# Performance work log

Measured on AMD Instinct MI355X. Metric: run time of the kernel, lower is better.

The kernel has to match this reference:

```python
import jax, jax.numpy as jnp
import numpy as np

B, S, DIM = 2, 2048, 2048
H = 16
NOPE, ROPE, VHD = 128, 64, 128
QKHD = NOPE + ROPE  # 192
KV_RANK = 512
EPS = 1e-5


def _rope(x, cos, sin):
    # x: [B,S,H,ROPE]; cos/sin: [S,ROPE//2]; torch view_as_complex pairs (even,odd)
    xr = x.reshape(*x.shape[:-1], ROPE // 2, 2)
    a, b = xr[..., 0], xr[..., 1]
    c = cos[None, :, None, :]
    s = sin[None, :, None, :]
    ra = a * c - b * s
    rb = a * s + b * c
    return jnp.stack([ra, rb], axis=-1).reshape(x.shape)


def setup_inputs() -> dict:
    key = jax.random.key(0)
    ks = jax.random.split(key, 12)
    std = 0.02
    x = jax.random.normal(ks[0], (B, S, DIM), jnp.float32)
    wq_w = jax.random.normal(ks[1], (DIM, H * QKHD), jnp.float32) * std
    wq_b = jnp.zeros((H * QKHD,), jnp.float32)
    wkv_a_w = jax.random.normal(ks[2], (DIM, KV_RANK + H * ROPE), jnp.float32) * std
    wkv_a_b = jnp.zeros((KV_RANK + H * ROPE,), jnp.float32)
    kvn_g = jnp.ones((KV_RANK,), jnp.float32)
    kvn_b = jnp.zeros((KV_RANK,), jnp.float32)
    wk_w = jax.random.normal(ks[3], (KV_RANK, H * NOPE), jnp.float32) * std
    wk_b = jnp.zeros((H * NOPE,), jnp.float32)
    wv_w = jax.random.normal(ks[4], (KV_RANK, H * VHD), jnp.float32) * std
    wv_b = jnp.zeros((H * VHD,), jnp.float32)
    wo_w = jax.random.normal(ks[5], (H * VHD, DIM), jnp.float32) * std
    wo_b = jnp.zeros((DIM,), jnp.float32)
    # RoPE tables: theta = pos / 10000^(2j/ROPE)
    inv_freq = 1.0 / (10000.0 ** (jnp.arange(0, ROPE, 2, dtype=jnp.float32) / ROPE))
    ang = jnp.arange(S, dtype=jnp.float32)[:, None] * inv_freq[None, :]  # [S, ROPE//2]
    cos, sin = jnp.cos(ang), jnp.sin(ang)
    mask = jnp.tril(jnp.ones((S, S), dtype=bool))
    return {"x": x, "wq_w": wq_w, "wq_b": wq_b, "wkv_a_w": wkv_a_w, "wkv_a_b": wkv_a_b,
            "kvn_g": kvn_g, "kvn_b": kvn_b, "wk_w": wk_w, "wk_b": wk_b,
            "wv_w": wv_w, "wv_b": wv_b, "wo_w": wo_w, "wo_b": wo_b,
            "cos": cos, "sin": sin, "mask": mask}


def reference(x, wq_w, wq_b, wkv_a_w, wkv_a_b, kvn_g, kvn_b, wk_w, wk_b,
              wv_w, wv_b, wo_w, wo_b, cos, sin, mask):
    # query projection (q_lora_rank == 0 path)
    q = x @ wq_w + wq_b                              # [B,S,H*QKHD]
    # low-rank kv: first H*ROPE dims are per-head k_rope, last KV_RANK is latent
    kv = x @ wkv_a_w + wkv_a_b                       # [B,S,KV_RANK+H*ROPE]
    k_rope = kv[..., : H * ROPE]
    c = kv[..., H * ROPE:]                           # latent [B,S,KV_RANK]
    mu = jnp.mean(c, axis=-1, keepdims=True)
    var = jnp.mean(jnp.square(c - mu), axis=-1, keepdims=True)
    c = (c - mu) / jnp.sqrt(var + EPS) * kvn_g + kvn_b
    k_nope = c @ wk_w + wk_b                         # [B,S,H*NOPE]
    v = c @ wv_w + wv_b                              # [B,S,H*VHD]
    # faithful to original: concat flat then view into heads
    k = jnp.concatenate([k_nope, k_rope], axis=-1).reshape(B, S, H, QKHD)
    q = q.reshape(B, S, H, QKHD)
    v = v.reshape(B, S, H, VHD)
    # RoPE on trailing ROPE dims
    q = jnp.concatenate([q[..., :NOPE], _rope(q[..., NOPE:], cos, sin)], axis=-1)
    k = jnp.concatenate([k[..., :NOPE], _rope(k[..., NOPE:], cos, sin)], axis=-1)
    scale = QKHD ** -0.5
    scores = jnp.einsum('bqhd,bkhd->bhqk', q, k) * scale
    scores = jnp.where(mask[None, None, :, :], scores, -jnp.inf)
    attn = jax.nn.softmax(scores, axis=-1)
    out = jnp.einsum('bhqk,bkhd->bqhd', attn, v).reshape(B, S, H * VHD)
    return out @ wo_w + wo_b
```

## Files before the change

### kernel.cpp

```cpp
#include <hip/hip_runtime.h>
#include <hip/hip_bf16.h>
#include <stdint.h>

#define B_ 2
#define S_ 2048
#define DIM_ 2048
#define H_ 16
#define M_ (B_*S_)

typedef __bf16 bf16x8 __attribute__((ext_vector_type(8)));
typedef float f32x4 __attribute__((ext_vector_type(4)));
typedef __hip_bfloat16 bf16;

__device__ __forceinline__ void async_copy16(const bf16* gsrc, bf16* ldst) {
  __builtin_amdgcn_global_load_lds((const __attribute__((address_space(1))) uint32_t*)gsrc,
                                   (__attribute__((address_space(3))) uint32_t*)ldst, 16, 0, 0);
}

__global__ void cvt_bf16_kernel(const float* __restrict__ in, bf16* __restrict__ out, int n) {
  int i = (blockIdx.x * 256 + threadIdx.x) * 4;
  if (i >= n) return;
  float4 v = *(const float4*)(in + i);
  bf16 o[4] = {__float2bfloat16(v.x), __float2bfloat16(v.y),
               __float2bfloat16(v.z), __float2bfloat16(v.w)};
  *(ushort4*)(out + i) = *(ushort4*)o;
}

__global__ void transpose_cvt_kernel(const float* __restrict__ W, bf16* __restrict__ Wt,
                                     int K, int N) {
  __shared__ float tile[32][33];
  int n0 = blockIdx.x * 32;
  int k0 = blockIdx.y * 32;
  int tx = threadIdx.x, ty = threadIdx.y;
  #pragma unroll
  for (int i = 0; i < 4; i++)
    tile[ty + i*8][tx] = W[(size_t)(k0 + ty + i*8) * N + n0 + tx];
  __syncthreads();
  #pragma unroll
  for (int i = 0; i < 4; i++)
    Wt[(size_t)(n0 + ty + i*8) * K + k0 + tx] = __float2bfloat16(tile[tx][ty + i*8]);
}

template <typename OutT, int MODE>
__global__ void __launch_bounds__(256) gemm_bt_kernel(
    const bf16* __restrict__ A, const bf16* __restrict__ Bt,
    const float* __restrict__ bias, const float* __restrict__ bias2,
    OutT* __restrict__ C, bf16* __restrict__ C2, bf16* __restrict__ C3,
    int M, int N, int K,
    const float* __restrict__ cosT, const float* __restrict__ sinT) {
  __shared__ bf16 As[128 * 32];
  __shared__ bf16 Bs[128 * 32];
  const int tid = threadIdx.x;
  const int wid = tid >> 6;
  const int lane = tid & 63;
  const int g = lane >> 4;
  const int c = lane & 15;

  int bx = blockIdx.x, by = blockIdx.y;
  {
    int gx = gridDim.x;
    int nwg = gx * gridDim.y;
    if ((nwg & 7) == 0) {
      int flat = by * gx + bx;
      int swz = (flat & 7) * (nwg >> 3) + (flat >> 3);
      bx = swz % gx;
      by = swz / gx;
    }
  }
  const int row0 = by * 128;
  const int col0 = bx * 128;
  const int wr = (wid >> 1) * 64;
  const int wc = (wid & 1) * 64;

  f32x4 acc[4][4] = {};

  const int srow = wid * 32 + (lane >> 2);
  const int scol = (lane & 3) * 8;
  const bf16* ga0 = A  + (size_t)(row0 + srow) * K + scol;
  const bf16* gb0 = Bt + (size_t)(col0 + srow) * K + scol;
  bf16* la0 = &As[(wid * 32) * 32];
  bf16* la1 = &As[(wid * 32 + 16) * 32];
  bf16* lb0 = &Bs[(wid * 32) * 32];
  bf16* lb1 = &Bs[(wid * 32 + 16) * 32];

  for (int k0 = 0; k0 < K; k0 += 32) {
    async_copy16(ga0 + k0, la0);
    async_copy16(ga0 + (size_t)16 * K + k0, la1);
    async_copy16(gb0 + k0, lb0);
    async_copy16(gb0 + (size_t)16 * K + k0, lb1);
    __syncthreads();
    bf16x8 af[4], bfr[4];
    #pragma unroll
    for (int i = 0; i < 4; i++) {
      af[i]  = *(const bf16x8*)&As[(wr + i*16 + c) * 32 + g*8];
      bfr[i] = *(const bf16x8*)&Bs[(wc + i*16 + c) * 32 + g*8];
    }
    #pragma unroll
    for (int mi = 0; mi < 4; mi++)
      #pragma unroll
      for (int ni = 0; ni < 4; ni++)
        acc[mi][ni] = __builtin_amdgcn_mfma_f32_16x16x32_bf16(af[mi], bfr[ni], acc[mi][ni], 0, 0, 0);
    __syncthreads();
  }

  if constexpr (MODE == 0) {
    #pragma unroll
    for (int mi = 0; mi < 4; mi++) {
      int row = row0 + wr + mi*16 + g*4;
      #pragma unroll
      for (int ni = 0; ni < 4; ni++) {
        int col = col0 + wc + ni*16 + c;
        float bv = bias[col];
        #pragma unroll
        for (int r = 0; r < 4; r++)
          C[(size_t)(row + r) * N + col] = acc[mi][ni][r] + bv;
      }
    }
  } else {
    auto rope_write = [&](bf16* __restrict__ dst, size_t obase, int s, int d,
                          float val[4], float scale) {
      if (d >= 128) {
        const int pp = (d - 128) >> 1;
        const bool even = (c & 1) == 0;
        #pragma unroll
        for (int r = 0; r < 4; r++) {
          float partner = __shfl_xor(val[r], 1);
          float a  = even ? val[r] : partner;
          float bb = even ? partner : val[r];
          float ct = cosT[(s + r) * 32 + pp], st = sinT[(s + r) * 32 + pp];
          float o = even ? (a * ct - bb * st) : (a * st + bb * ct);
          dst[obase + (size_t)r * 192] = __float2bfloat16(o * scale);
        }
      } else {
        #pragma unroll
        for (int r = 0; r < 4; r++)
          dst[obase + (size_t)r * 192] = __float2bfloat16(val[r] * scale);
      }
    };

    #pragma unroll
    for (int mi = 0; mi < 4; mi++) {
      int row = row0 + wr + mi*16 + g*4;
      int s = row & (S_ - 1);
      int b = row >> 11;
      #pragma unroll
      for (int ni = 0; ni < 4; ni++) {
        int col = col0 + wc + ni*16 + c;
        float val[4];
        if constexpr (MODE == 6) {
          if (col < 3072) {
            float bv = bias[col];
            #pragma unroll
            for (int r = 0; r < 4; r++) val[r] = acc[mi][ni][r] + bv;
            int h = col / 192;
            int d = col - h * 192;
            size_t obase = ((size_t)(b * H_ + h) * S_ + s) * 192 + d;
            rope_write((bf16*)C, obase, s, d, val, 0.07216878364870323f);
          } else {
            int cc = col - 3072;
            float bv = bias2[cc];
            #pragma unroll
            for (int r = 0; r < 4; r++) val[r] = acc[mi][ni][r] + bv;
            if (cc < 1024) {
              int flat = 2048 + cc;
              int h = flat / 192;
              int d = flat - h * 192;
              size_t obase = ((size_t)(b * H_ + h) * S_ + s) * 192 + d;
              rope_write(C2, obase, s, d, val, 1.0f);
            } else {
              #pragma unroll
              for (int r = 0; r < 4; r++)
                C3[(size_t)(row + r) * 512 + (cc - 1024)] = __float2bfloat16(val[r]);
            }
          }
        } else {
          if (col < 2048) {
            float bv = bias[col];
            #pragma unroll
            for (int r = 0; r < 4; r++) val[r] = acc[mi][ni][r] + bv;
            int h = col / 192;
            int d = col - h * 192;
            size_t obase = ((size_t)(b * H_ + h) * S_ + s) * 192 + d;
            rope_write((bf16*)C, obase, s, d, val, 1.0f);
          } else {
            int cc = col - 2048;
            float bv = bias2[cc];
            bf16 tmp[4];
            #pragma unroll
            for (int r = 0; r < 4; r++) tmp[r] = __float2bfloat16(acc[mi][ni][r] + bv);
            size_t idx = ((size_t)(b * H_ + (cc >> 7)) * 128 + (cc & 127)) * S_ + s;
            *(ushort4*)&C2[idx] = *(ushort4*)tmp;
          }
        }
      }
    }
  }
}

__global__ void __launch_bounds__(256) layernorm_kernel(
    const bf16* __restrict__ craw,
    const float* __restrict__ gamma, const float* __restrict__ beta,
    bf16* __restrict__ cn) {
  int row = blockIdx.x * 4 + (threadIdx.x >> 6);
  int lane = threadIdx.x & 63;
  bf16x8 v = *(const bf16x8*)(craw + (size_t)row * 512 + lane * 8);
  float f[8], sum = 0.f, sq = 0.f;
  #pragma unroll
  for (int j = 0; j < 8; j++) { f[j] = (float)v[j]; sum += f[j]; sq += f[j]*f[j]; }
  #pragma unroll
  for (int d = 1; d < 64; d <<= 1) {
    sum += __shfl_xor(sum, d);
    sq  += __shfl_xor(sq, d);
  }
  float mu = sum * (1.f/512.f);
  float var = sq * (1.f/512.f) - mu*mu;
  float rstd = rsqrtf(var + 1e-5f);
  bf16x8 ov;
  #pragma unroll
  for (int j = 0; j < 8; j++) {
    int col = lane*8 + j;
    float o = (f[j] - mu) * rstd * gamma[col] + beta[col];
    ov[j] = (__bf16)o;
  }
  *(bf16x8*)(cn + (size_t)row * 512 + lane * 8) = ov;
}

__global__ void __launch_bounds__(256) flash_attn_kernel(
    const bf16* __restrict__ Qa, const bf16* __restrict__ Ka,
    const bf16* __restrict__ Vt, bf16* __restrict__ Oa) {
  __shared__ bf16 Ks[64 * 200];
  __shared__ bf16 Vs[128 * 72];
  __shared__ bf16 Ps[4][16 * 72];
  const int tid = threadIdx.x;
  const int wid = tid >> 6, lane = tid & 63;
  const int g = lane >> 4, c = lane & 15;
  const int bh = blockIdx.y;
  const int qt = gridDim.x - 1 - blockIdx.x;
  const int q0 = qt * 64;
  const int qw = q0 + wid * 16;
  const float NEG_INF = -__builtin_inff();

  bf16x8 qf[6];
  {
    const bf16* qrow = Qa + ((size_t)bh * S_ + qw + c) * 192;
    #pragma unroll
    for (int t = 0; t < 6; t++) qf[t] = *(const bf16x8*)(qrow + t*32 + g*8);
  }
  float m = NEG_INF, lsum = 0.f;
  f32x4 o[8] = {};

  const int kr = tid >> 2, kpart = tid & 3;
  const int vdv = tid >> 1, vhalf = tid & 1;

  for (int kt = 0; kt <= qt; kt++) {
    const int kv0 = kt * 64;
    {
      const bf16* src = Ka + ((size_t)bh * S_ + kv0 + kr) * 192;
      #pragma unroll
      for (int j = 0; j < 6; j++) {
        int col = (kpart + 4*j) * 8;
        *(bf16x8*)&Ks[kr * 200 + col] = *(const bf16x8*)(src + col);
      }
      const bf16* vsrc = Vt + ((size_t)bh * 128 + vdv) * S_ + kv0;
      #pragma unroll
      for (int j = 0; j < 4; j++) {
        int col = (vhalf*4 + j) * 8;
        *(bf16x8*)&Vs[vdv * 72 + col] = *(const bf16x8*)(vsrc + col);
      }
    }
    __syncthreads();

    f32x4 sc[4] = {};
    #pragma unroll
    for (int mb = 0; mb < 4; mb++) {
      #pragma unroll
      for (int t = 0; t < 6; t++) {
        bf16x8 kf = *(const bf16x8*)&Ks[(mb*16 + c) * 200 + t*32 + g*8];
        sc[mb] = __builtin_amdgcn_mfma_f32_16x16x32_bf16(kf, qf[t], sc[mb], 0, 0, 0);
      }
    }
    if (kt == qt) {
      #pragma unroll
      for (int mb = 0; mb < 4; mb++)
        #pragma unroll
        for (int r = 0; r < 4; r++)
          if (kv0 + mb*16 + g*4 + r > qw + c) sc[mb][r] = NEG_INF;
    }
    float pm = NEG_INF;
    #pragma unroll
    for (int mb = 0; mb < 4; mb++)
      #pragma unroll
      for (int r = 0; r < 4; r++) pm = fmaxf(pm, sc[mb][r]);
    pm = fmaxf(pm, __shfl_xor(pm, 16));
    pm = fmaxf(pm, __shfl_xor(pm, 32));
    const float newm = fmaxf(m, pm);
    const float alpha = __expf(m - newm);
    float rs = 0.f;
    float pv[4][4];
    #pragma unroll
    for (int mb = 0; mb < 4; mb++)
      #pragma unroll
      for (int r = 0; r < 4; r++) { pv[mb][r] = __expf(sc[mb][r] - newm); rs += pv[mb][r]; }
    rs += __shfl_xor(rs, 16);
    rs += __shfl_xor(rs, 32);
    lsum = lsum * alpha + rs;
    m = newm;
    #pragma unroll
    for (int mb = 0; mb < 4; mb++) {
      bf16 w[4];
      #pragma unroll
      for (int r = 0; r < 4; r++) w[r] = __float2bfloat16(pv[mb][r]);
      *(ushort4*)&Ps[wid][c * 72 + mb*16 + g*4] = *(ushort4*)w;
    }
    __syncthreads();
    float ar[4];
    #pragma unroll
    for (int r = 0; r < 4; r++) ar[r] = __shfl(alpha, 20*g + r);
    #pragma unroll
    for (int nb = 0; nb < 8; nb++)
      #pragma unroll
      for (int r = 0; r < 4; r++) o[nb][r] *= ar[r];
    #pragma unroll
    for (int t2 = 0; t2 < 2; t2++) {
      bf16x8 pa = *(const bf16x8*)&Ps[wid][c * 72 + t2*32 + g*8];
      #pragma unroll
      for (int nb = 0; nb < 8; nb++) {
        bf16x8 vf = *(const bf16x8*)&Vs[(nb*16 + c) * 72 + t2*32 + g*8];
        o[nb] = __builtin_amdgcn_mfma_f32_16x16x32_bf16(pa, vf, o[nb], 0, 0, 0);
      }
    }
    __syncthreads();
  }

  float lr[4];
  #pragma unroll
  for (int r = 0; r < 4; r++) lr[r] = 1.f / __shfl(lsum, 20*g + r);
  const int b = bh >> 4, h = bh & 15;
  #pragma unroll
  for (int nb = 0; nb < 8; nb++) {
    #pragma unroll
    for (int r = 0; r < 4; r++) {
      int srow = qw + g*4 + r;
      int dv = nb*16 + c;
      Oa[(((size_t)(b * S_ + srow)) * H_ + h) * 128 + dv] = __float2bfloat16(o[nb][r] * lr[r]);
    }
  }
}

extern "C" void kernel_launch(void* const* d_in, const int* in_sizes, int n_in,
                              void* d_out, int out_size, void* d_ws, size_t ws_size,
                              hipStream_t stream) {
  const float* x     = (const float*)d_in[0];
  const float* wq_w  = (const float*)d_in[1];
  const float* wq_b  = (const float*)d_in[2];
  const float* wkv_w = (const float*)d_in[3];
  const float* wkv_b = (const float*)d_in[4];
  const float* kvn_g = (const float*)d_in[5];
  const float* kvn_b = (const float*)d_in[6];
  const float* wk_w  = (const float*)d_in[7];
  const float* wk_b  = (const float*)d_in[8];
  const float* wv_w  = (const float*)d_in[9];
  const float* wv_b  = (const float*)d_in[10];
  const float* wo_w  = (const float*)d_in[11];
  const float* wo_b  = (const float*)d_in[12];
  const float* cosT  = (const float*)d_in[13];
  const float* sinT  = (const float*)d_in[14];
  float* out = (float*)d_out;
  (void)in_sizes; (void)n_in; (void)out_size; (void)ws_size;

  char* p = (char*)d_ws;
  auto alloc = [&](size_t elems) { bf16* r = (bf16*)p; p += elems * 2; return r; };
  bf16* xb      = alloc((size_t)M_ * 2048);
  bf16* wqkv_t  = alloc((size_t)4608 * 2048);
  bf16* wkv2_t  = alloc((size_t)4096 * 512);
  bf16* wo_t    = alloc((size_t)2048 * 2048);
  bf16* c_raw   = alloc((size_t)M_ * 512);
  bf16* cn      = alloc((size_t)M_ * 512);
  bf16* q_at    = alloc((size_t)M_ * 3072);
  bf16* k_at    = alloc((size_t)M_ * 3072);
  bf16* v_at    = alloc((size_t)M_ * 2048);
  bf16* att_o   = alloc((size_t)M_ * 2048);

  cvt_bf16_kernel<<<dim3((M_*2048)/1024), 256, 0, stream>>>(x, xb, M_*2048);
  transpose_cvt_kernel<<<dim3(3072/32, 2048/32), dim3(32,8), 0, stream>>>(wq_w,  wqkv_t,                      2048, 3072);
  transpose_cvt_kernel<<<dim3(1536/32, 2048/32), dim3(32,8), 0, stream>>>(wkv_w, wqkv_t + (size_t)3072*2048, 2048, 1536);
  transpose_cvt_kernel<<<dim3(2048/32, 512/32),  dim3(32,8), 0, stream>>>(wk_w,  wkv2_t,                     512,  2048);
  transpose_cvt_kernel<<<dim3(2048/32, 512/32),  dim3(32,8), 0, stream>>>(wv_w,  wkv2_t + (size_t)2048*512,  512,  2048);
  transpose_cvt_kernel<<<dim3(2048/32, 2048/32), dim3(32,8), 0, stream>>>(wo_w,  wo_t,                       2048, 2048);
  gemm_bt_kernel<bf16,6><<<dim3(4608/128, M_/128), 256, 0, stream>>>(
      xb, wqkv_t, wq_b, wkv_b, q_at, k_at, c_raw, M_, 4608, 2048, cosT, sinT);
  layernorm_kernel<<<dim3(M_/4), 256, 0, stream>>>(c_raw, kvn_g, kvn_b, cn);
  gemm_bt_kernel<bf16,7><<<dim3(4096/128, M_/128), 256, 0, stream>>>(
      cn, wkv2_t, wk_b, wv_b, k_at, v_at, nullptr, M_, 4096, 512, cosT, sinT);
  flash_attn_kernel<<<dim3(S_/64, B_*H_), 256, 0, stream>>>(q_at, k_at, v_at, att_o);
  gemm_bt_kernel<float,0><<<dim3(2048/128, M_/128), 256, 0, stream>>>(
      att_o, wo_t, wo_b, nullptr, out, nullptr, nullptr, M_, 2048, 2048, nullptr, nullptr);
}
```

Measured before the change: 581.3 us.

## Enlarge flash-attention query tile to 128 rows and prefetch K/V through registers

Each attention block now handles 128 query rows, with every wave owning two 16-row groups, so each K/V tile loaded into LDS is reused by twice as many queries. The next K/V tile is loaded from global memory into registers while the current tile is computed, then written to LDS between barriers. The intra-loop barrier between P store and PV matmul is dropped, and launch bounds request two blocks per CU. The cost is higher register pressure from doubled accumulators and staging registers, and half as many blocks in the grid.

```diff
diff --git a/kernel.cpp b/kernel.cpp
--- a/kernel.cpp
+++ b/kernel.cpp
@@ -225,124 +225,146 @@
   *(bf16x8*)(cn + (size_t)row * 512 + lane * 8) = ov;
 }
 
-__global__ void __launch_bounds__(256) flash_attn_kernel(
+__global__ void __launch_bounds__(256, 2) flash_attn_kernel(
     const bf16* __restrict__ Qa, const bf16* __restrict__ Ka,
     const bf16* __restrict__ Vt, bf16* __restrict__ Oa) {
   __shared__ bf16 Ks[64 * 200];
   __shared__ bf16 Vs[128 * 72];
-  __shared__ bf16 Ps[4][16 * 72];
+  __shared__ bf16 Ps[4][32 * 72];
   const int tid = threadIdx.x;
   const int wid = tid >> 6, lane = tid & 63;
   const int g = lane >> 4, c = lane & 15;
   const int bh = blockIdx.y;
   const int qt = gridDim.x - 1 - blockIdx.x;
-  const int q0 = qt * 64;
-  const int qw = q0 + wid * 16;
+  const int q0 = qt * 128;
+  const int qw = q0 + wid * 32;
   const float NEG_INF = -__builtin_inff();
 
-  bf16x8 qf[6];
-  {
-    const bf16* qrow = Qa + ((size_t)bh * S_ + qw + c) * 192;
-    #pragma unroll
-    for (int t = 0; t < 6; t++) qf[t] = *(const bf16x8*)(qrow + t*32 + g*8);
-  }
-  float m = NEG_INF, lsum = 0.f;
-  f32x4 o[8] = {};
+  bf16x8 qf[2][6];
+  #pragma unroll
+  for (int rg = 0; rg < 2; rg++) {
+    const bf16* qrow = Qa + ((size_t)bh * S_ + qw + rg*16 + c) * 192;
+    #pragma unroll
+    for (int t = 0; t < 6; t++) qf[rg][t] = *(const bf16x8*)(qrow + t*32 + g*8);
+  }
+  float m[2] = {NEG_INF, NEG_INF}, lsum[2] = {0.f, 0.f};
+  f32x4 o[2][8] = {};
 
   const int kr = tid >> 2, kpart = tid & 3;
   const int vdv = tid >> 1, vhalf = tid & 1;
 
-  for (int kt = 0; kt <= qt; kt++) {
+  bf16x8 kst[6], vst[4];
+  const int nkt = 2*qt + 2;
+
+  auto load_regs = [&](int kt) {
+    const bf16* src = Ka + ((size_t)bh * S_ + kt*64 + kr) * 192;
+    #pragma unroll
+    for (int j = 0; j < 6; j++) kst[j] = *(const bf16x8*)(src + (kpart + 4*j) * 8);
+    const bf16* vsrc = Vt + ((size_t)bh * 128 + vdv) * S_ + kt*64;
+    #pragma unroll
+    for (int j = 0; j < 4; j++) vst[j] = *(const bf16x8*)(vsrc + (vhalf*4 + j) * 8);
+  };
+  auto write_lds = [&]() {
+    #pragma unroll
+    for (int j = 0; j < 6; j++) *(bf16x8*)&Ks[kr * 200 + (kpart + 4*j) * 8] = kst[j];
+    #pragma unroll
+    for (int j = 0; j < 4; j++) *(bf16x8*)&Vs[vdv * 72 + (vhalf*4 + j) * 8] = vst[j];
+  };
+
+  load_regs(0);
+  write_lds();
+  __syncthreads();
+
+  for (int kt = 0; kt < nkt; kt++) {
     const int kv0 = kt * 64;
-    {
-      const bf16* src = Ka + ((size_t)bh * S_ + kv0 + kr) * 192;
-      #pragma unroll
-      for (int j = 0; j < 6; j++) {
-        int col = (kpart + 4*j) * 8;
-        *(bf16x8*)&Ks[kr * 200 + col] = *(const bf16x8*)(src + col);
-      }
-      const bf16* vsrc = Vt + ((size_t)bh * 128 + vdv) * S_ + kv0;
-      #pragma unroll
-      for (int j = 0; j < 4; j++) {
-        int col = (vhalf*4 + j) * 8;
-        *(bf16x8*)&Vs[vdv * 72 + col] = *(const bf16x8*)(vsrc + col);
-      }
-    }
-    __syncthreads();
-
-    f32x4 sc[4] = {};
-    #pragma unroll
-    for (int mb = 0; mb < 4; mb++) {
-      #pragma unroll
-      for (int t = 0; t < 6; t++) {
-        bf16x8 kf = *(const bf16x8*)&Ks[(mb*16 + c) * 200 + t*32 + g*8];
-        sc[mb] = __builtin_amdgcn_mfma_f32_16x16x32_bf16(kf, qf[t], sc[mb], 0, 0, 0);
-      }
-    }
-    if (kt == qt) {
+    if (kt + 1 < nkt) load_regs(kt + 1);
+
+    #pragma unroll
+    for (int rg = 0; rg < 2; rg++) {
+      const int qbase = qw + rg * 16;
+      if (kv0 > qbase + 15) continue;
+
+      f32x4 sc[4] = {};
+      #pragma unroll
+      for (int mb = 0; mb < 4; mb++) {
+        #pragma unroll
+        for (int t = 0; t < 6; t++) {
+          bf16x8 kf = *(const bf16x8*)&Ks[(mb*16 + c) * 200 + t*32 + g*8];
+          sc[mb] = __builtin_amdgcn_mfma_f32_16x16x32_bf16(kf, qf[rg][t], sc[mb], 0, 0, 0);
+        }
+      }
+      if (kv0 + 63 > qbase) {
+        #pragma unroll
+        for (int mb = 0; mb < 4; mb++)
+          #pragma unroll
+          for (int r = 0; r < 4; r++)
+            if (kv0 + mb*16 + g*4 + r > qbase + c) sc[mb][r] = NEG_INF;
+      }
+      float pm = NEG_INF;
       #pragma unroll
       for (int mb = 0; mb < 4; mb++)
         #pragma unroll
-        for (int r = 0; r < 4; r++)
-          if (kv0 + mb*16 + g*4 + r > qw + c) sc[mb][r] = NEG_INF;
-    }
-    float pm = NEG_INF;
-    #pragma unroll
-    for (int mb = 0; mb < 4; mb++)
-      #pragma unroll
-      for (int r = 0; r < 4; r++) pm = fmaxf(pm, sc[mb][r]);
-    pm = fmaxf(pm, __shfl_xor(pm, 16));
-    pm = fmaxf(pm, __shfl_xor(pm, 32));
-    const float newm = fmaxf(m, pm);
-    const float alpha = __expf(m - newm);
-    float rs = 0.f;
-    float pv[4][4];
-    #pragma unroll
-    for (int mb = 0; mb < 4; mb++)
-      #pragma unroll
-      for (int r = 0; r < 4; r++) { pv[mb][r] = __expf(sc[mb][r] - newm); rs += pv[mb][r]; }
-    rs += __shfl_xor(rs, 16);
-    rs += __shfl_xor(rs, 32);
-    lsum = lsum * alpha + rs;
-    m = newm;
-    #pragma unroll
-    for (int mb = 0; mb < 4; mb++) {
-      bf16 w[4];
-      #pragma unroll
-      for (int r = 0; r < 4; r++) w[r] = __float2bfloat16(pv[mb][r]);
-      *(ushort4*)&Ps[wid][c * 72 + mb*16 + g*4] = *(ushort4*)w;
-    }
-    __syncthreads();
-    float ar[4];
-    #pragma unroll
-    for (int r = 0; r < 4; r++) ar[r] = __shfl(alpha, 20*g + r);
-    #pragma unroll
-    for (int nb = 0; nb < 8; nb++)
-      #pragma unroll
-      for (int r = 0; r < 4; r++) o[nb][r] *= ar[r];
-    #pragma unroll
-    for (int t2 = 0; t2 < 2; t2++) {
-      bf16x8 pa = *(const bf16x8*)&Ps[wid][c * 72 + t2*32 + g*8];
-      #pragma unroll
-      for (int nb = 0; nb < 8; nb++) {
-        bf16x8 vf = *(const bf16x8*)&Vs[(nb*16 + c) * 72 + t2*32 + g*8];
-        o[nb] = __builtin_amdgcn_mfma_f32_16x16x32_bf16(pa, vf, o[nb], 0, 0, 0);
-      }
-    }
-    __syncthreads();
-  }
-
-  float lr[4];
-  #pragma unroll
-  for (int r = 0; r < 4; r++) lr[r] = 1.f / __shfl(lsum, 20*g + r);
+        for (int r = 0; r < 4; r++) pm = fmaxf(pm, sc[mb][r]);
+      pm = fmaxf(pm, __shfl_xor(pm, 16));
+      pm = fmaxf(pm, __shfl_xor(pm, 32));
+      const float newm = fmaxf(m[rg], pm);
+      const float alpha = __expf(m[rg] - newm);
+      float rs = 0.f;
+      float pv[4][4];
+      #pragma unroll
+      for (int mb = 0; mb < 4; mb++)
+        #pragma unroll
+        for (int r = 0; r < 4; r++) { pv[mb][r] = __expf(sc[mb][r] - newm); rs += pv[mb][r]; }
+      rs += __shfl_xor(rs, 16);
+      rs += __shfl_xor(rs, 32);
+      lsum[rg] = lsum[rg] * alpha + rs;
+      m[rg] = newm;
+      #pragma unroll
+      for (int mb = 0; mb < 4; mb++) {
+        bf16 w[4];
+        #pragma unroll
+        for (int r = 0; r < 4; r++) w[r] = __float2bfloat16(pv[mb][r]);
+        *(ushort4*)&Ps[wid][(rg*16 + c) * 72 + mb*16 + g*4] = *(ushort4*)w;
+      }
+      float ar[4];
+      #pragma unroll
+      for (int r = 0; r < 4; r++) ar[r] = __shfl(alpha, 20*g + r);
+      #pragma unroll
+      for (int nb = 0; nb < 8; nb++)
+        #pragma unroll
+        for (int r = 0; r < 4; r++) o[rg][nb][r] *= ar[r];
+      #pragma unroll
+      for (int t2 = 0; t2 < 2; t2++) {
+        bf16x8 pa = *(const bf16x8*)&Ps[wid][(rg*16 + c) * 72 + t2*32 + g*8];
+        #pragma unroll
+        for (int nb = 0; nb < 8; nb++) {
+          bf16x8 vf = *(const bf16x8*)&Vs[(nb*16 + c) * 72 + t2*32 + g*8];
+          o[rg][nb] = __builtin_amdgcn_mfma_f32_16x16x32_bf16(pa, vf, o[rg][nb], 0, 0, 0);
+        }
+      }
+    }
+
+    if (kt + 1 < nkt) {
+      __syncthreads();
+      write_lds();
+      __syncthreads();
+    }
+  }
+
   const int b = bh >> 4, h = bh & 15;
   #pragma unroll
-  for (int nb = 0; nb < 8; nb++) {
-    #pragma unroll
-    for (int r = 0; r < 4; r++) {
-      int srow = qw + g*4 + r;
-      int dv = nb*16 + c;
-      Oa[(((size_t)(b * S_ + srow)) * H_ + h) * 128 + dv] = __float2bfloat16(o[nb][r] * lr[r]);
+  for (int rg = 0; rg < 2; rg++) {
+    float lr[4];
+    #pragma unroll
+    for (int r = 0; r < 4; r++) lr[r] = 1.f / __shfl(lsum[rg], 20*g + r);
+    #pragma unroll
+    for (int nb = 0; nb < 8; nb++) {
+      #pragma unroll
+      for (int r = 0; r < 4; r++) {
+        int srow = qw + rg*16 + g*4 + r;
+        int dv = nb*16 + c;
+        Oa[(((size_t)(b * S_ + srow)) * H_ + h) * 128 + dv] = __float2bfloat16(o[rg][nb][r] * lr[r]);
+      }
     }
   }
 }
@@ -392,7 +414,7 @@
   layernorm_kernel<<<dim3(M_/4), 256, 0, stream>>>(c_raw, kvn_g, kvn_b, cn);
   gemm_bt_kernel<bf16,7><<<dim3(4096/128, M_/128), 256, 0, stream>>>(
       cn, wkv2_t, wk_b, wv_b, k_at, v_at, nullptr, M_, 4096, 512, cosT, sinT);
-  flash_attn_kernel<<<dim3(S_/64, B_*H_), 256, 0, stream>>>(q_at, k_at, v_at, att_o);
+  flash_attn_kernel<<<dim3(S_/128, B_*H_), 256, 0, stream>>>(q_at, k_at, v_at, att_o);
   gemm_bt_kernel<float,0><<<dim3(2048/128, M_/128), 256, 0, stream>>>(
       att_o, wo_t, wo_b, nullptr, out, nullptr, nullptr, M_, 2048, 2048, nullptr, nullptr);
 }
```

New measurement: 538.0 us. 7.5% less time.
